# Optimization experiments

Hardware: AMD Instinct MI355X
Metric: run time of the kernel (lower is better)

Reference implementation:

```python
import jax, jax.numpy as jnp
import numpy as np

D_MODEL = 512
N_HEADS = 8
HEAD_DIM = D_MODEL // N_HEADS
MAX_LEN = 250  # relative table has 2*MAX_LEN-1 = 499 rows
B, L = 2, 2048


def setup_inputs() -> dict:
    rng = jax.random.key(0)
    ks = jax.random.split(rng, 10)
    w = 1.0 / np.sqrt(D_MODEL)
    return {
        "query": jax.random.normal(ks[0], (B, L, D_MODEL), jnp.float32),
        "key": jax.random.normal(ks[1], (B, L, D_MODEL), jnp.float32),
        "value": jax.random.normal(ks[2], (B, L, D_MODEL), jnp.float32),
        "mask": jax.random.randint(ks[3], (B, L), 0, 2, jnp.int32),
        # weights stored as [in, out]; apply as x @ W + b (equivalent to torch Linear)
        "Wq": jax.random.normal(ks[4], (D_MODEL, D_MODEL), jnp.float32) * w,
        "bq": jnp.zeros((D_MODEL,), jnp.float32),
        "Wk": jax.random.normal(ks[5], (D_MODEL, D_MODEL), jnp.float32) * w,
        "bk": jnp.zeros((D_MODEL,), jnp.float32),
        "Wv": jax.random.normal(ks[6], (D_MODEL, D_MODEL), jnp.float32) * w,
        "bv": jnp.zeros((D_MODEL,), jnp.float32),
        "Wo": jax.random.normal(ks[7], (D_MODEL, D_MODEL), jnp.float32) * w,
        "bo": jnp.zeros((D_MODEL,), jnp.float32),
        "rel_table": jax.random.normal(ks[8], (2 * MAX_LEN - 1, HEAD_DIM), jnp.float32),
    }


def reference(query, key, value, mask, Wq, bq, Wk, bk, Wv, bv, Wo, bo, rel_table):
    b, l, d = query.shape
    hd = d // N_HEADS

    def split_heads(x):  # [b,l,d] -> [b,h,l,hd]
        return x.reshape(b, l, N_HEADS, hd).transpose(0, 2, 1, 3)

    Q = split_heads(query @ Wq + bq)
    K = split_heads(key @ Wk + bk)
    V = split_heads(value @ Wv + bv)

    scores = jnp.einsum('bhid,bhjd->bhij', Q, K) / jnp.sqrt(jnp.float32(hd))

    # relative position indices: idx[i,j] = clamp(j - i + MAX_LEN-1, 0, 2*MAX_LEN-2)
    pos = jnp.arange(l)
    idx = jnp.clip(pos[None, :] - pos[:, None] + MAX_LEN - 1, 0, 2 * MAX_LEN - 2)
    rel = rel_table[idx]  # [l, l, hd] gather
    # Shaw-style additive relative-position bias (per-pair scalar from Q . rel)
    scores = scores + jnp.einsum('bhid,ijd->bhij', Q, rel)

    # key-padding mask: [b,l] -> [b,1,1,l]
    scores = jnp.where(mask[:, None, None, :] == 0, jnp.float32(-1e10), scores)

    weights = jax.nn.softmax(scores, axis=-1)  # [b,h,l,l]
    out = jnp.einsum('bhij,bhjd->bhid', weights, V)
    out = out.transpose(0, 2, 1, 3).reshape(b, l, d)
    return out @ Wo + bo
```

## Files before the change

kernel.cpp:

```cpp
#include <hip/hip_runtime.h>
#include <math.h>

#define NREL 499
#define NREL_PAD 500
#define LDB 72
#define LDT 72

typedef __attribute__((ext_vector_type(8))) short bf16x8;
typedef __attribute__((ext_vector_type(4))) float f32x4;

__device__ __forceinline__ float bf2f(ushort x) {
  union { unsigned u; float f; } v; v.u = ((unsigned)x) << 16; return v.f;
}
__device__ __forceinline__ ushort f2bf(float x) {
  union { float f; unsigned u; } v; v.f = x;
  return (ushort)((v.u + 0x8000u) >> 16);
}
__device__ __forceinline__ bf16x8 pack8(float4 a, float4 b) {
  bf16x8 r;
  r[0] = (short)f2bf(a.x); r[1] = (short)f2bf(a.y);
  r[2] = (short)f2bf(a.z); r[3] = (short)f2bf(a.w);
  r[4] = (short)f2bf(b.x); r[5] = (short)f2bf(b.y);
  r[6] = (short)f2bf(b.z); r[7] = (short)f2bf(b.w);
  return r;
}

__global__ __launch_bounds__(256) void prep_wt(const float* __restrict__ W0,
                                               const float* __restrict__ W1,
                                               const float* __restrict__ W2,
                                               const float* __restrict__ W3,
                                               const int* __restrict__ mask,
                                               ushort* __restrict__ Wt,
                                               ushort* __restrict__ maskbf) {
  __shared__ float T[64][68];
  const int t = threadIdx.x;
  const int k0 = blockIdx.x * 64, n0 = blockIdx.y * 64, z = blockIdx.z;
  const float* W = (z == 0) ? W0 : (z == 1) ? W1 : (z == 2) ? W2 : W3;
#pragma unroll
  for (int s = 0; s < 4; ++s) {
    int idx = t + s * 256;
    int r = idx >> 4, c4 = (idx & 15) << 2;
    *(float4*)&T[r][c4] = *(const float4*)(W + (size_t)(k0 + r) * 512 + n0 + c4);
  }
  if (blockIdx.x == 0 && blockIdx.y == 0) {
    int base = z * 1024 + t * 4;
    int4 mv = *(const int4*)(mask + base);
    ushort4 mo;
    mo.x = mv.x ? 0x3F80 : 0; mo.y = mv.y ? 0x3F80 : 0;
    mo.z = mv.z ? 0x3F80 : 0; mo.w = mv.w ? 0x3F80 : 0;
    *(ushort4*)(maskbf + base) = mo;
  }
  __syncthreads();
#pragma unroll
  for (int s = 0; s < 4; ++s) {
    int idx = t + s * 256;
    int row = idx >> 4, c4 = (idx & 15) << 2;
    ushort4 u = make_ushort4(f2bf(T[c4 + 0][row]), f2bf(T[c4 + 1][row]),
                             f2bf(T[c4 + 2][row]), f2bf(T[c4 + 3][row]));
    *(ushort4*)(Wt + (size_t)z * 262144 + (size_t)(n0 + row) * 512 + k0 + c4) = u;
  }
}

template <int MODE, int AFP32>
__device__ __forceinline__ void gemm_tile_body(const void* __restrict__ Av,
                                               const ushort* __restrict__ Wt,
                                               const float* __restrict__ bias,
                                               const int* __restrict__ mvec,
                                               void* __restrict__ outv,
                                               int bx, int by, float oscale) {
  __shared__ ushort As[64 * LDT];
  __shared__ ushort Bs[64 * LDT];
  const int t = threadIdx.x;
  const int lane = t & 63, wave = t >> 6;
  const int m16 = lane & 15, quad = lane >> 4;
  const int koff = quad << 3;
  const int i0 = by * 64, n0 = bx * 64;
  const int row0 = t >> 3, off0 = (t & 7) << 3;
  const int row1 = (t + 256) >> 3, off1 = ((t + 256) & 7) << 3;
  const ushort* Ab16 = (const ushort*)Av + (size_t)i0 * 512;
  const float*  Ab32 = (const float*)Av + (size_t)i0 * 512;
  const ushort* Bb = Wt + (size_t)n0 * 512;

  uint4 ar0, ar1;
  float4 af00, af01, af10, af11;
  if (AFP32) {
    af00 = *(const float4*)(Ab32 + (size_t)row0 * 512 + off0);
    af01 = *(const float4*)(Ab32 + (size_t)row0 * 512 + off0 + 4);
    af10 = *(const float4*)(Ab32 + (size_t)row1 * 512 + off1);
    af11 = *(const float4*)(Ab32 + (size_t)row1 * 512 + off1 + 4);
  } else {
    ar0 = *(const uint4*)(Ab16 + (size_t)row0 * 512 + off0);
    ar1 = *(const uint4*)(Ab16 + (size_t)row1 * 512 + off1);
  }
  uint4 br0 = *(const uint4*)(Bb + (size_t)row0 * 512 + off0);
  uint4 br1 = *(const uint4*)(Bb + (size_t)row1 * 512 + off1);

  f32x4 acc[4] = {{0.f, 0.f, 0.f, 0.f}, {0.f, 0.f, 0.f, 0.f},
                  {0.f, 0.f, 0.f, 0.f}, {0.f, 0.f, 0.f, 0.f}};

  for (int ks = 0; ks < 8; ++ks) {
    __syncthreads();
    if (AFP32) {
      *(bf16x8*)&As[row0 * LDT + off0] = pack8(af00, af01);
      *(bf16x8*)&As[row1 * LDT + off1] = pack8(af10, af11);
    } else {
      *(uint4*)&As[row0 * LDT + off0] = ar0;
      *(uint4*)&As[row1 * LDT + off1] = ar1;
    }
    *(uint4*)&Bs[row0 * LDT + off0] = br0;
    *(uint4*)&Bs[row1 * LDT + off1] = br1;
    __syncthreads();

    const int kn = ((ks + 1) & 7) << 6;
    if (AFP32) {
      af00 = *(const float4*)(Ab32 + (size_t)row0 * 512 + kn + off0);
      af01 = *(const float4*)(Ab32 + (size_t)row0 * 512 + kn + off0 + 4);
      af10 = *(const float4*)(Ab32 + (size_t)row1 * 512 + kn + off1);
      af11 = *(const float4*)(Ab32 + (size_t)row1 * 512 + kn + off1 + 4);
    } else {
      ar0 = *(const uint4*)(Ab16 + (size_t)row0 * 512 + kn + off0);
      ar1 = *(const uint4*)(Ab16 + (size_t)row1 * 512 + kn + off1);
    }
    br0 = *(const uint4*)(Bb + (size_t)row0 * 512 + kn + off0);
    br1 = *(const uint4*)(Bb + (size_t)row1 * 512 + kn + off1);

    __builtin_amdgcn_s_setprio(1);
    if (MODE != 1) {
#pragma unroll
      for (int kh = 0; kh < 2; ++kh) {
        bf16x8 af = *(const bf16x8*)&As[((wave << 4) + m16) * LDT + (kh << 5) + koff];
#pragma unroll
        for (int nt = 0; nt < 4; ++nt) {
          bf16x8 wf = *(const bf16x8*)&Bs[((nt << 4) + m16) * LDT + (kh << 5) + koff];
          acc[nt] = __builtin_amdgcn_mfma_f32_16x16x32_bf16(af, wf, acc[nt], 0, 0, 0);
        }
      }
    } else {
#pragma unroll
      for (int kh = 0; kh < 2; ++kh) {
        bf16x8 wf = *(const bf16x8*)&Bs[((wave << 4) + m16) * LDT + (kh << 5) + koff];
#pragma unroll
        for (int it = 0; it < 4; ++it) {
          bf16x8 af = *(const bf16x8*)&As[((it << 4) + m16) * LDT + (kh << 5) + koff];
          acc[it] = __builtin_amdgcn_mfma_f32_16x16x32_bf16(wf, af, acc[it], 0, 0, 0);
        }
      }
    }
    __builtin_amdgcn_s_setprio(0);
  }

  if (MODE == 0) {
    float* out = (float*)outv;
#pragma unroll
    for (int nt = 0; nt < 4; ++nt) {
      float bn = bias[n0 + (nt << 4) + m16];
#pragma unroll
      for (int r = 0; r < 4; ++r) {
        int i = i0 + (wave << 4) + (quad << 2) + r;
        out[(size_t)i * 512 + n0 + (nt << 4) + m16] = acc[nt][r] + bn;
      }
    }
  } else if (MODE == 2) {
    ushort* out = (ushort*)outv;
    const int b = i0 >> 11, l0 = i0 & 2047, h = n0 >> 6;
#pragma unroll
    for (int nt = 0; nt < 4; ++nt) {
      float bn = bias[n0 + (nt << 4) + m16];
      int d = (nt << 4) + m16;
#pragma unroll
      for (int r = 0; r < 4; ++r) {
        int il = (wave << 4) + (quad << 2) + r;
        out[((size_t)(b * 8 + h) * 2048 + l0 + il) * 64 + d] =
            f2bf((acc[nt][r] + bn) * oscale);
      }
    }
  } else {
    ushort* out = (ushort*)outv;
    const int b = i0 >> 11, l0 = i0 & 2047, h = n0 >> 6;
    float4 b4 = *(const float4*)(bias + n0 + (wave << 4) + (quad << 2));
    float bb[4] = {b4.x, b4.y, b4.z, b4.w};
    float mkf[4];
#pragma unroll
    for (int it = 0; it < 4; ++it)
      mkf[it] = (mvec[b * 2048 + l0 + (it << 4) + m16] != 0) ? 1.f : 0.f;
#pragma unroll
    for (int r = 0; r < 4; ++r) {
      int d = (wave << 4) + (quad << 2) + r;
#pragma unroll
      for (int it = 0; it < 4; ++it) {
        out[((size_t)(b * 8 + h) * 64 + d) * 2048 + l0 + (it << 4) + m16] =
            f2bf((acc[it][r] + bb[r]) * mkf[it]);
      }
    }
  }
}

template <int MODE, int AFP32>
__global__ __launch_bounds__(256) void gemm_tile(const void* __restrict__ A,
                                                 const ushort* __restrict__ Wt,
                                                 const float* __restrict__ bias,
                                                 void* __restrict__ outv) {
  gemm_tile_body<MODE, AFP32>(A, Wt, bias, nullptr, outv, blockIdx.x,
                              blockIdx.y, 1.f);
}

__global__ __launch_bounds__(256) void gemm_qkv(
    const float* __restrict__ q, const float* __restrict__ k,
    const float* __restrict__ v, const ushort* __restrict__ Wt,
    const float* __restrict__ bq, const float* __restrict__ bk,
    const float* __restrict__ bv, const int* __restrict__ mask,
    ushort* __restrict__ Qw, ushort* __restrict__ Kw, ushort* __restrict__ Vtw) {
  const int z = blockIdx.z;
  if (z == 0) {
    gemm_tile_body<2, 1>(q, Wt, bq, nullptr, (void*)Qw, blockIdx.x, blockIdx.y,
                         0.125f);
  } else if (z == 1) {
    gemm_tile_body<2, 1>(k, Wt + 262144, bk, nullptr, (void*)Kw, blockIdx.x,
                         blockIdx.y, 1.f);
  } else {
    gemm_tile_body<1, 1>(v, Wt + 2 * 262144, bv, mask, (void*)Vtw, blockIdx.x,
                         blockIdx.y, 1.f);
  }
}

__global__ __launch_bounds__(256) void qrel_mfma(const ushort* __restrict__ Qw,
                                                 const float* __restrict__ rel,
                                                 float* __restrict__ qrel) {
  const int t = threadIdx.x;
  const int lane = t & 63, wave = t >> 6;
  const int m16 = lane & 15, quad = lane >> 4;
  const int r0 = blockIdx.x * 64;
  const int i0 = blockIdx.y * 64;
  const int bh = blockIdx.z;
  const ushort* Qb = Qw + ((size_t)bh * 2048 + i0 + (wave << 4) + m16) * 64;
  bf16x8 qa0 = *(const bf16x8*)(Qb + (quad << 3));
  bf16x8 qa1 = *(const bf16x8*)(Qb + 32 + (quad << 3));

  f32x4 acc[4] = {{0.f, 0.f, 0.f, 0.f}, {0.f, 0.f, 0.f, 0.f},
                  {0.f, 0.f, 0.f, 0.f}, {0.f, 0.f, 0.f, 0.f}};
#pragma unroll
  for (int rt = 0; rt < 4; ++rt) {
    int rr = min(r0 + (rt << 4) + m16, NREL - 1);
    const float* rp = rel + (size_t)rr * 64 + (quad << 3);
    float4 a0 = *(const float4*)rp,        a1 = *(const float4*)(rp + 4);
    float4 a2 = *(const float4*)(rp + 32), a3 = *(const float4*)(rp + 36);
    a0.x *= 8.f; a0.y *= 8.f; a0.z *= 8.f; a0.w *= 8.f;
    a1.x *= 8.f; a1.y *= 8.f; a1.z *= 8.f; a1.w *= 8.f;
    a2.x *= 8.f; a2.y *= 8.f; a2.z *= 8.f; a2.w *= 8.f;
    a3.x *= 8.f; a3.y *= 8.f; a3.z *= 8.f; a3.w *= 8.f;
    bf16x8 rf0 = pack8(a0, a1);
    bf16x8 rf1 = pack8(a2, a3);
    acc[rt] = __builtin_amdgcn_mfma_f32_16x16x32_bf16(qa0, rf0, acc[rt], 0, 0, 0);
    acc[rt] = __builtin_amdgcn_mfma_f32_16x16x32_bf16(qa1, rf1, acc[rt], 0, 0, 0);
  }
#pragma unroll
  for (int rt = 0; rt < 4; ++rt) {
    int r = r0 + (rt << 4) + m16;
    if (r < NREL_PAD) {
#pragma unroll
      for (int rg = 0; rg < 4; ++rg) {
        int i = i0 + (wave << 4) + (quad << 2) + rg;
        qrel[((size_t)bh * 2048 + i) * NREL_PAD + r] = acc[rt][rg];
      }
    }
  }
}

__device__ __forceinline__ void gather_qv(float qv[4][4],
                                          const float* __restrict__ qrow,
                                          float e_lo, float e_hi,
                                          int iq, int iw0, int j0, int quad) {
  if (j0 - iw0 >= 264) {
#pragma unroll
    for (int jt = 0; jt < 4; ++jt)
#pragma unroll
      for (int r = 0; r < 4; ++r) qv[jt][r] = e_hi;
  } else if (iw0 - j0 >= 312) {
#pragma unroll
    for (int jt = 0; jt < 4; ++jt)
#pragma unroll
      for (int r = 0; r < 4; ++r) qv[jt][r] = e_lo;
  } else {
#pragma unroll
    for (int jt = 0; jt < 4; ++jt) {
#pragma unroll
      for (int r = 0; r < 4; ++r) {
        int j = j0 + (jt << 4) + (quad << 2) + r;
        int rr = min(NREL - 1, max(0, j - iq + 249));
        qv[jt][r] = qrow[rr];
      }
    }
  }
}

template <int SPLIT>
__global__ __launch_bounds__(256) void flash_attn(
    const ushort* __restrict__ Qw, const ushort* __restrict__ Kw,
    const ushort* __restrict__ Vt, const float* __restrict__ qrel,
    const ushort* __restrict__ maskbf, ushort* __restrict__ attnbf,
    float* __restrict__ Opart, float* __restrict__ MLp) {
  __shared__ ushort QPs[64 * LDB];
  __shared__ ushort Ks[64 * LDB];
  __shared__ ushort Vs[64 * LDB];
  const int t = threadIdx.x;
  const int lane = t & 63, wave = t >> 6;
  const int m16 = lane & 15, quad = lane >> 4;
  const int koff = quad << 3;
  const int bid = ((int)blockIdx.y << 5) + (int)blockIdx.x;
  const int swz = ((bid & 7) << 6) + (bid >> 3);
  const int i0 = (swz & 31) << 6;
  const int bh = swz >> 5;
  const int b = bh >> 3, h = bh & 7;
  const int jstart = SPLIT ? ((int)blockIdx.z << 10) : 0;
  const int jend = SPLIT ? (jstart + 1024) : 2048;
  const ushort* Qb = Qw + (size_t)bh * 2048 * 64;
  const ushort* Kb = Kw + (size_t)bh * 2048 * 64;
  const ushort* Vb = Vt + (size_t)bh * 64 * 2048;
  const ushort* mbf = maskbf + b * 2048;
  const int iw0 = i0 + (wave << 4);
  const int iq = iw0 + m16;
  const float* qrow = qrel + ((size_t)bh * 2048 + iq) * NREL_PAD;
  const float e_lo = qrow[0], e_hi = qrow[NREL - 1];

  const int row0 = t >> 3, off0 = (t & 7) << 3;
  const int row1 = (t + 256) >> 3, off1 = ((t + 256) & 7) << 3;

  *(uint4*)&QPs[row0 * LDB + off0] =
      *(const uint4*)(Qb + (size_t)(i0 + row0) * 64 + off0);
  *(uint4*)&QPs[row1 * LDB + off1] =
      *(const uint4*)(Qb + (size_t)(i0 + row1) * 64 + off1);
  __syncthreads();

  bf16x8 qa0 = *(const bf16x8*)&QPs[((wave << 4) + m16) * LDB + koff];
  bf16x8 qa1 = *(const bf16x8*)&QPs[((wave << 4) + m16) * LDB + 32 + koff];

  uint4 kr0 = *(const uint4*)(Kb + (size_t)(jstart + row0) * 64 + off0);
  uint4 kr1 = *(const uint4*)(Kb + (size_t)(jstart + row1) * 64 + off1);
  uint4 vr0 = *(const uint4*)(Vb + (size_t)row0 * 2048 + jstart + off0);
  uint4 vr1 = *(const uint4*)(Vb + (size_t)row1 * 2048 + jstart + off1);
  bf16x8 mfr0 = *(const bf16x8*)(mbf + jstart + koff);
  bf16x8 mfr1 = *(const bf16x8*)(mbf + jstart + 32 + koff);
  float qv[4][4];
  gather_qv(qv, qrow, e_lo, e_hi, iq, iw0, jstart, quad);

  float m_i = -INFINITY;
  f32x4 oacc[4];
  f32x4 lacc = {0.f, 0.f, 0.f, 0.f};
#pragma unroll
  for (int dt = 0; dt < 4; ++dt) oacc[dt] = (f32x4){0.f, 0.f, 0.f, 0.f};

  for (int j0 = jstart; j0 < jend; j0 += 64) {
    __syncthreads();
    *(uint4*)&Ks[row0 * LDB + off0] = kr0;
    *(uint4*)&Ks[row1 * LDB + off1] = kr1;
    *(uint4*)&Vs[row0 * LDB + off0] = vr0;
    *(uint4*)&Vs[row1 * LDB + off1] = vr1;
    __syncthreads();

    const int jn = (j0 + 64 < jend) ? (j0 + 64) : jstart;
    uint4 kn0 = *(const uint4*)(Kb + (size_t)(jn + row0) * 64 + off0);
    uint4 kn1 = *(const uint4*)(Kb + (size_t)(jn + row1) * 64 + off1);
    uint4 vn0 = *(const uint4*)(Vb + (size_t)row0 * 2048 + jn + off0);
    uint4 vn1 = *(const uint4*)(Vb + (size_t)row1 * 2048 + jn + off1);
    bf16x8 mfn0 = *(const bf16x8*)(mbf + jn + koff);
    bf16x8 mfn1 = *(const bf16x8*)(mbf + jn + 32 + koff);
    float qn[4][4];
    gather_qv(qn, qrow, e_lo, e_hi, iq, iw0, jn, quad);

    f32x4 sacc[4];
    __builtin_amdgcn_s_setprio(1);
#pragma unroll
    for (int jt = 0; jt < 4; ++jt) {
      bf16x8 kb0 = *(const bf16x8*)&Ks[((jt << 4) + m16) * LDB + koff];
      bf16x8 kb1 = *(const bf16x8*)&Ks[((jt << 4) + m16) * LDB + 32 + koff];
      f32x4 z = {qv[jt][0], qv[jt][1], qv[jt][2], qv[jt][3]};
      z = __builtin_amdgcn_mfma_f32_16x16x32_bf16(kb0, qa0, z, 0, 0, 0);
      z = __builtin_amdgcn_mfma_f32_16x16x32_bf16(kb1, qa1, z, 0, 0, 0);
      sacc[jt] = z;
    }
    __builtin_amdgcn_s_setprio(0);

    float t0 = fmaxf(fmaxf(sacc[0][0], sacc[0][1]), fmaxf(sacc[0][2], sacc[0][3]));
    float t1 = fmaxf(fmaxf(sacc[1][0], sacc[1][1]), fmaxf(sacc[1][2], sacc[1][3]));
    float t2 = fmaxf(fmaxf(sacc[2][0], sacc[2][1]), fmaxf(sacc[2][2], sacc[2][3]));
    float t3 = fmaxf(fmaxf(sacc[3][0], sacc[3][1]), fmaxf(sacc[3][2], sacc[3][3]));
    float mx = fmaxf(fmaxf(t0, t1), fmaxf(t2, t3));
    mx = fmaxf(mx, __shfl_xor(mx, 16));
    mx = fmaxf(mx, __shfl_xor(mx, 32));

    if (__any(mx > m_i + 8.f)) {
      float mnew = fmaxf(m_i, mx);
      float al = __expf(m_i - mnew);
      m_i = mnew;
#pragma unroll
      for (int dt = 0; dt < 4; ++dt)
#pragma unroll
        for (int r = 0; r < 4; ++r) oacc[dt][r] *= al;
#pragma unroll
      for (int r = 0; r < 4; ++r) lacc[r] *= al;
    }

    const int prow = ((wave << 4) + m16) * LDB;
#pragma unroll
    for (int jt = 0; jt < 4; ++jt) {
      ushort4 pk;
      pk.x = f2bf(__expf(sacc[jt][0] - m_i));
      pk.y = f2bf(__expf(sacc[jt][1] - m_i));
      pk.z = f2bf(__expf(sacc[jt][2] - m_i));
      pk.w = f2bf(__expf(sacc[jt][3] - m_i));
      *(ushort4*)&QPs[prow + (jt << 4) + (quad << 2)] = pk;
    }
    __asm__ volatile("s_waitcnt lgkmcnt(0)" ::: "memory");

    bf16x8 pa0 = *(const bf16x8*)&QPs[prow + koff];
    bf16x8 pa1 = *(const bf16x8*)&QPs[prow + 32 + koff];
    __builtin_amdgcn_s_setprio(1);
    lacc = __builtin_amdgcn_mfma_f32_16x16x32_bf16(mfr0, pa0, lacc, 0, 0, 0);
    lacc = __builtin_amdgcn_mfma_f32_16x16x32_bf16(mfr1, pa1, lacc, 0, 0, 0);
#pragma unroll
    for (int dt = 0; dt < 4; ++dt) {
      bf16x8 vb0 = *(const bf16x8*)&Vs[((dt << 4) + m16) * LDB + koff];
      bf16x8 vb1 = *(const bf16x8*)&Vs[((dt << 4) + m16) * LDB + 32 + koff];
      oacc[dt] = __builtin_amdgcn_mfma_f32_16x16x32_bf16(vb0, pa0, oacc[dt], 0, 0, 0);
      oacc[dt] = __builtin_amdgcn_mfma_f32_16x16x32_bf16(vb1, pa1, oacc[dt], 0, 0, 0);
    }
    __builtin_amdgcn_s_setprio(0);

    kr0 = kn0; kr1 = kn1; vr0 = vn0; vr1 = vn1;
    mfr0 = mfn0; mfr1 = mfn1;
#pragma unroll
    for (int jt = 0; jt < 4; ++jt)
#pragma unroll
      for (int r = 0; r < 4; ++r) qv[jt][r] = qn[jt][r];
  }

  if (SPLIT) {
    const size_t rb = ((size_t)(((int)blockIdx.z << 4) + bh) * 2048 + iq);
    float* dst = Opart + rb * 64;
#pragma unroll
    for (int dt = 0; dt < 4; ++dt) {
      float4 st;
      st.x = oacc[dt][0]; st.y = oacc[dt][1];
      st.z = oacc[dt][2]; st.w = oacc[dt][3];
      *(float4*)(dst + (dt << 4) + (quad << 2)) = st;
    }
    if (quad == 0) { MLp[rb * 2] = m_i; MLp[rb * 2 + 1] = lacc[0]; }
  } else {
    float inv = 1.0f / lacc[0];
    ushort* dst = attnbf + (size_t)(b * 2048 + iq) * 512 + h * 64;
#pragma unroll
    for (int dt = 0; dt < 4; ++dt) {
      ushort4 st;
      st.x = f2bf(oacc[dt][0] * inv);
      st.y = f2bf(oacc[dt][1] * inv);
      st.z = f2bf(oacc[dt][2] * inv);
      st.w = f2bf(oacc[dt][3] * inv);
      *(ushort4*)(dst + (dt << 4) + (quad << 2)) = st;
    }
  }
}

__global__ __launch_bounds__(256) void combine_attn(
    const float* __restrict__ Opart, const float* __restrict__ MLp,
    ushort* __restrict__ attnbf) {
  const int t = threadIdx.x;
  const int i0 = blockIdx.x * 64, bh = blockIdx.y;
  const int b = bh >> 3, h = bh & 7;
  const int row = t >> 2, d0 = (t & 3) << 4;
  const int i = i0 + row;
  const size_t rb0 = (size_t)bh * 2048 + i;
  const size_t rb1 = (size_t)(16 + bh) * 2048 + i;
  float m0 = MLp[rb0 * 2], l0 = MLp[rb0 * 2 + 1];
  float m1 = MLp[rb1 * 2], l1 = MLp[rb1 * 2 + 1];
  float M = fmaxf(m0, m1);
  float w0 = __expf(m0 - M), w1 = __expf(m1 - M);
  float inv = 1.0f / (w0 * l0 + w1 * l1);
  const float* p0 = Opart + rb0 * 64 + d0;
  const float* p1 = Opart + rb1 * 64 + d0;
  ushort* dst = attnbf + ((size_t)(b * 2048) + i) * 512 + h * 64 + d0;
#pragma unroll
  for (int c = 0; c < 4; ++c) {
    float4 a = *(const float4*)(p0 + c * 4);
    float4 q = *(const float4*)(p1 + c * 4);
    ushort4 o;
    o.x = f2bf((w0 * a.x + w1 * q.x) * inv);
    o.y = f2bf((w0 * a.y + w1 * q.y) * inv);
    o.z = f2bf((w0 * a.z + w1 * q.z) * inv);
    o.w = f2bf((w0 * a.w + w1 * q.w) * inv);
    *(ushort4*)(dst + c * 4) = o;
  }
}

extern "C" void kernel_launch(void* const* d_in, const int* in_sizes, int n_in,
                              void* d_out, int out_size, void* d_ws,
                              size_t ws_size, hipStream_t stream) {
  const float* query = (const float*)d_in[0];
  const float* key   = (const float*)d_in[1];
  const float* value = (const float*)d_in[2];
  const int*   mask  = (const int*)d_in[3];
  const float* Wq = (const float*)d_in[4];
  const float* bq = (const float*)d_in[5];
  const float* Wk = (const float*)d_in[6];
  const float* bk = (const float*)d_in[7];
  const float* Wv = (const float*)d_in[8];
  const float* bv = (const float*)d_in[9];
  const float* Wo = (const float*)d_in[10];
  const float* bo = (const float*)d_in[11];
  const float* rel = (const float*)d_in[12];

  char* w = (char*)d_ws;
  size_t off = 0;
  ushort* Qw  = (ushort*)(w + off); off += (size_t)16 * 2048 * 64 * 2;
  ushort* Kw  = (ushort*)(w + off); off += (size_t)16 * 2048 * 64 * 2;
  ushort* Vtw = (ushort*)(w + off); off += (size_t)16 * 64 * 2048 * 2;
  ushort* Wt  = (ushort*)(w + off); off += (size_t)4 * 512 * 512 * 2;
  float* qrel = (float*)(w + off);  off += (size_t)16 * 2048 * NREL_PAD * 4;
  ushort* attnbf = (ushort*)(w + off); off += (size_t)4096 * 512 * 2;
  ushort* maskbf = (ushort*)(w + off); off += (size_t)2 * 2048 * 2 + 8160;
  float* Opart = (float*)(w + off); off += (size_t)2 * 16 * 2048 * 64 * 4;
  float* MLp  = (float*)(w + off);  off += (size_t)2 * 16 * 2048 * 2 * 4;
  float* out = (float*)d_out;
  const bool split = (ws_size >= off);

  dim3 bb(256);
  hipLaunchKernelGGL(prep_wt, dim3(8, 8, 4), bb, 0, stream, Wq, Wk, Wv, Wo,
                     mask, Wt, maskbf);
  hipLaunchKernelGGL(gemm_qkv, dim3(8, 64, 3), bb, 0, stream, query, key, value,
                     Wt, bq, bk, bv, mask, Qw, Kw, Vtw);
  hipLaunchKernelGGL(qrel_mfma, dim3(8, 32, 16), bb, 0, stream, Qw, rel, qrel);
  if (split) {
    hipLaunchKernelGGL((flash_attn<1>), dim3(32, 16, 2), bb, 0, stream, Qw, Kw,
                       Vtw, qrel, maskbf, attnbf, Opart, MLp);
    hipLaunchKernelGGL(combine_attn, dim3(32, 16), bb, 0, stream, Opart, MLp,
                       attnbf);
  } else {
    hipLaunchKernelGGL((flash_attn<0>), dim3(32, 16), bb, 0, stream, Qw, Kw,
                       Vtw, qrel, maskbf, attnbf, (float*)attnbf,
                       (float*)attnbf);
  }
  hipLaunchKernelGGL((gemm_tile<0, 0>), dim3(8, 64), bb, 0, stream, attnbf,
                     Wt + 3 * 262144, bo, (void*)out);
}
```

Measured before the change: 242.6 us.

## Drop split-KV flash attention and stage bf16 rel table through LDS in qrel

Precomputes a bf16, pre-scaled copy of the relative-position table in the weight-prep kernel. The qrel kernel then loads Q and rel tiles into shared memory with coalesced loads, replacing per-lane fp32 loads and conversions. The split-KV flash attention path and its combine kernel are removed in favour of a single unsplit pass, eliminating the partial-output writes and the extra launch. The trade-off is half as many attention blocks, which may reduce GPU occupancy.

```diff
diff --git a/kernel.cpp b/kernel.cpp
--- a/kernel.cpp
+++ b/kernel.cpp
@@ -30,8 +30,10 @@
                                                const float* __restrict__ W2,
                                                const float* __restrict__ W3,
                                                const int* __restrict__ mask,
+                                               const float* __restrict__ rel,
                                                ushort* __restrict__ Wt,
-                                               ushort* __restrict__ maskbf) {
+                                               ushort* __restrict__ maskbf,
+                                               ushort* __restrict__ rel8) {
   __shared__ float T[64][68];
   const int t = threadIdx.x;
   const int k0 = blockIdx.x * 64, n0 = blockIdx.y * 64, z = blockIdx.z;
@@ -49,6 +51,22 @@
     mo.x = mv.x ? 0x3F80 : 0; mo.y = mv.y ? 0x3F80 : 0;
     mo.z = mv.z ? 0x3F80 : 0; mo.w = mv.w ? 0x3F80 : 0;
     *(ushort4*)(maskbf + base) = mo;
+  } else if (blockIdx.x == 1 && blockIdx.y == 0) {
+    int base = z * 8192 + t * 32;
+#pragma unroll
+    for (int c = 0; c < 4; ++c) {
+      ushort4 o;
+      int e0 = base + c * 8;
+      ushort tmp[8];
+#pragma unroll
+      for (int k = 0; k < 8; ++k) {
+        int e = e0 + k;
+        float v = (e < NREL * 64) ? rel[e] * 8.f : 0.f;
+        tmp[k] = f2bf(v);
+      }
+      *(ushort4*)(rel8 + e0) = make_ushort4(tmp[0], tmp[1], tmp[2], tmp[3]);
+      *(ushort4*)(rel8 + e0 + 4) = make_ushort4(tmp[4], tmp[5], tmp[6], tmp[7]);
+    }
   }
   __syncthreads();
 #pragma unroll
@@ -223,44 +241,51 @@
   }
 }
 
-__global__ __launch_bounds__(256) void qrel_mfma(const ushort* __restrict__ Qw,
-                                                 const float* __restrict__ rel,
+__global__ __launch_bounds__(256) void qrel_tile(const ushort* __restrict__ Qw,
+                                                 const ushort* __restrict__ rel8,
                                                  float* __restrict__ qrel) {
+  __shared__ ushort As[64 * LDT];
+  __shared__ ushort Bs[64 * LDT];
   const int t = threadIdx.x;
   const int lane = t & 63, wave = t >> 6;
   const int m16 = lane & 15, quad = lane >> 4;
+  const int koff = quad << 3;
   const int r0 = blockIdx.x * 64;
   const int i0 = blockIdx.y * 64;
   const int bh = blockIdx.z;
-  const ushort* Qb = Qw + ((size_t)bh * 2048 + i0 + (wave << 4) + m16) * 64;
-  bf16x8 qa0 = *(const bf16x8*)(Qb + (quad << 3));
-  bf16x8 qa1 = *(const bf16x8*)(Qb + 32 + (quad << 3));
+  const int row0 = t >> 3, off0 = (t & 7) << 3;
+  const int row1 = (t + 256) >> 3, off1 = ((t + 256) & 7) << 3;
+
+  *(uint4*)&As[row0 * LDT + off0] =
+      *(const uint4*)(Qw + ((size_t)bh * 2048 + i0 + row0) * 64 + off0);
+  *(uint4*)&As[row1 * LDT + off1] =
+      *(const uint4*)(Qw + ((size_t)bh * 2048 + i0 + row1) * 64 + off1);
+  *(uint4*)&Bs[row0 * LDT + off0] =
+      *(const uint4*)(rel8 + (size_t)(r0 + row0) * 64 + off0);
+  *(uint4*)&Bs[row1 * LDT + off1] =
+      *(const uint4*)(rel8 + (size_t)(r0 + row1) * 64 + off1);
+  __syncthreads();
 
   f32x4 acc[4] = {{0.f, 0.f, 0.f, 0.f}, {0.f, 0.f, 0.f, 0.f},
                   {0.f, 0.f, 0.f, 0.f}, {0.f, 0.f, 0.f, 0.f}};
 #pragma unroll
-  for (int rt = 0; rt < 4; ++rt) {
-    int rr = min(r0 + (rt << 4) + m16, NREL - 1);
-    const float* rp = rel + (size_t)rr * 64 + (quad << 3);
-    float4 a0 = *(const float4*)rp,        a1 = *(const float4*)(rp + 4);
-    float4 a2 = *(const float4*)(rp + 32), a3 = *(const float4*)(rp + 36);
-    a0.x *= 8.f; a0.y *= 8.f; a0.z *= 8.f; a0.w *= 8.f;
-    a1.x *= 8.f; a1.y *= 8.f; a1.z *= 8.f; a1.w *= 8.f;
-    a2.x *= 8.f; a2.y *= 8.f; a2.z *= 8.f; a2.w *= 8.f;
-    a3.x *= 8.f; a3.y *= 8.f; a3.z *= 8.f; a3.w *= 8.f;
-    bf16x8 rf0 = pack8(a0, a1);
-    bf16x8 rf1 = pack8(a2, a3);
-    acc[rt] = __builtin_amdgcn_mfma_f32_16x16x32_bf16(qa0, rf0, acc[rt], 0, 0, 0);
-    acc[rt] = __builtin_amdgcn_mfma_f32_16x16x32_bf16(qa1, rf1, acc[rt], 0, 0, 0);
-  }
-#pragma unroll
-  for (int rt = 0; rt < 4; ++rt) {
-    int r = r0 + (rt << 4) + m16;
+  for (int kh = 0; kh < 2; ++kh) {
+    bf16x8 af = *(const bf16x8*)&As[((wave << 4) + m16) * LDT + (kh << 5) + koff];
+#pragma unroll
+    for (int nt = 0; nt < 4; ++nt) {
+      bf16x8 wf = *(const bf16x8*)&Bs[((nt << 4) + m16) * LDT + (kh << 5) + koff];
+      acc[nt] = __builtin_amdgcn_mfma_f32_16x16x32_bf16(af, wf, acc[nt], 0, 0, 0);
+    }
+  }
+
+#pragma unroll
+  for (int nt = 0; nt < 4; ++nt) {
+    int r = r0 + (nt << 4) + m16;
     if (r < NREL_PAD) {
 #pragma unroll
       for (int rg = 0; rg < 4; ++rg) {
         int i = i0 + (wave << 4) + (quad << 2) + rg;
-        qrel[((size_t)bh * 2048 + i) * NREL_PAD + r] = acc[rt][rg];
+        qrel[((size_t)bh * 2048 + i) * NREL_PAD + r] = acc[nt][rg];
       }
     }
   }
@@ -293,12 +318,10 @@
   }
 }
 
-template <int SPLIT>
 __global__ __launch_bounds__(256) void flash_attn(
     const ushort* __restrict__ Qw, const ushort* __restrict__ Kw,
     const ushort* __restrict__ Vt, const float* __restrict__ qrel,
-    const ushort* __restrict__ maskbf, ushort* __restrict__ attnbf,
-    float* __restrict__ Opart, float* __restrict__ MLp) {
+    const ushort* __restrict__ maskbf, ushort* __restrict__ attnbf) {
   __shared__ ushort QPs[64 * LDB];
   __shared__ ushort Ks[64 * LDB];
   __shared__ ushort Vs[64 * LDB];
@@ -311,8 +334,6 @@
   const int i0 = (swz & 31) << 6;
   const int bh = swz >> 5;
   const int b = bh >> 3, h = bh & 7;
-  const int jstart = SPLIT ? ((int)blockIdx.z << 10) : 0;
-  const int jend = SPLIT ? (jstart + 1024) : 2048;
   const ushort* Qb = Qw + (size_t)bh * 2048 * 64;
   const ushort* Kb = Kw + (size_t)bh * 2048 * 64;
   const ushort* Vb = Vt + (size_t)bh * 64 * 2048;
@@ -334,14 +355,14 @@
   bf16x8 qa0 = *(const bf16x8*)&QPs[((wave << 4) + m16) * LDB + koff];
   bf16x8 qa1 = *(const bf16x8*)&QPs[((wave << 4) + m16) * LDB + 32 + koff];
 
-  uint4 kr0 = *(const uint4*)(Kb + (size_t)(jstart + row0) * 64 + off0);
-  uint4 kr1 = *(const uint4*)(Kb + (size_t)(jstart + row1) * 64 + off1);
-  uint4 vr0 = *(const uint4*)(Vb + (size_t)row0 * 2048 + jstart + off0);
-  uint4 vr1 = *(const uint4*)(Vb + (size_t)row1 * 2048 + jstart + off1);
-  bf16x8 mfr0 = *(const bf16x8*)(mbf + jstart + koff);
-  bf16x8 mfr1 = *(const bf16x8*)(mbf + jstart + 32 + koff);
+  uint4 kr0 = *(const uint4*)(Kb + (size_t)row0 * 64 + off0);
+  uint4 kr1 = *(const uint4*)(Kb + (size_t)row1 * 64 + off1);
+  uint4 vr0 = *(const uint4*)(Vb + (size_t)row0 * 2048 + off0);
+  uint4 vr1 = *(const uint4*)(Vb + (size_t)row1 * 2048 + off1);
+  bf16x8 mfr0 = *(const bf16x8*)(mbf + koff);
+  bf16x8 mfr1 = *(const bf16x8*)(mbf + 32 + koff);
   float qv[4][4];
-  gather_qv(qv, qrow, e_lo, e_hi, iq, iw0, jstart, quad);
+  gather_qv(qv, qrow, e_lo, e_hi, iq, iw0, 0, quad);
 
   float m_i = -INFINITY;
   f32x4 oacc[4];
@@ -349,7 +370,7 @@
 #pragma unroll
   for (int dt = 0; dt < 4; ++dt) oacc[dt] = (f32x4){0.f, 0.f, 0.f, 0.f};
 
-  for (int j0 = jstart; j0 < jend; j0 += 64) {
+  for (int j0 = 0; j0 < 2048; j0 += 64) {
     __syncthreads();
     *(uint4*)&Ks[row0 * LDB + off0] = kr0;
     *(uint4*)&Ks[row1 * LDB + off1] = kr1;
@@ -357,7 +378,7 @@
     *(uint4*)&Vs[row1 * LDB + off1] = vr1;
     __syncthreads();
 
-    const int jn = (j0 + 64 < jend) ? (j0 + 64) : jstart;
+    const int jn = (j0 + 64) & 2047;
     uint4 kn0 = *(const uint4*)(Kb + (size_t)(jn + row0) * 64 + off0);
     uint4 kn1 = *(const uint4*)(Kb + (size_t)(jn + row1) * 64 + off1);
     uint4 vn0 = *(const uint4*)(Vb + (size_t)row0 * 2048 + jn + off0);
@@ -434,60 +455,16 @@
       for (int r = 0; r < 4; ++r) qv[jt][r] = qn[jt][r];
   }
 
-  if (SPLIT) {
-    const size_t rb = ((size_t)(((int)blockIdx.z << 4) + bh) * 2048 + iq);
-    float* dst = Opart + rb * 64;
-#pragma unroll
-    for (int dt = 0; dt < 4; ++dt) {
-      float4 st;
-      st.x = oacc[dt][0]; st.y = oacc[dt][1];
-      st.z = oacc[dt][2]; st.w = oacc[dt][3];
-      *(float4*)(dst + (dt << 4) + (quad << 2)) = st;
-    }
-    if (quad == 0) { MLp[rb * 2] = m_i; MLp[rb * 2 + 1] = lacc[0]; }
-  } else {
-    float inv = 1.0f / lacc[0];
-    ushort* dst = attnbf + (size_t)(b * 2048 + iq) * 512 + h * 64;
-#pragma unroll
-    for (int dt = 0; dt < 4; ++dt) {
-      ushort4 st;
-      st.x = f2bf(oacc[dt][0] * inv);
-      st.y = f2bf(oacc[dt][1] * inv);
-      st.z = f2bf(oacc[dt][2] * inv);
-      st.w = f2bf(oacc[dt][3] * inv);
-      *(ushort4*)(dst + (dt << 4) + (quad << 2)) = st;
-    }
-  }
-}
-
-__global__ __launch_bounds__(256) void combine_attn(
-    const float* __restrict__ Opart, const float* __restrict__ MLp,
-    ushort* __restrict__ attnbf) {
-  const int t = threadIdx.x;
-  const int i0 = blockIdx.x * 64, bh = blockIdx.y;
-  const int b = bh >> 3, h = bh & 7;
-  const int row = t >> 2, d0 = (t & 3) << 4;
-  const int i = i0 + row;
-  const size_t rb0 = (size_t)bh * 2048 + i;
-  const size_t rb1 = (size_t)(16 + bh) * 2048 + i;
-  float m0 = MLp[rb0 * 2], l0 = MLp[rb0 * 2 + 1];
-  float m1 = MLp[rb1 * 2], l1 = MLp[rb1 * 2 + 1];
-  float M = fmaxf(m0, m1);
-  float w0 = __expf(m0 - M), w1 = __expf(m1 - M);
-  float inv = 1.0f / (w0 * l0 + w1 * l1);
-  const float* p0 = Opart + rb0 * 64 + d0;
-  const float* p1 = Opart + rb1 * 64 + d0;
-  ushort* dst = attnbf + ((size_t)(b * 2048) + i) * 512 + h * 64 + d0;
-#pragma unroll
-  for (int c = 0; c < 4; ++c) {
-    float4 a = *(const float4*)(p0 + c * 4);
-    float4 q = *(const float4*)(p1 + c * 4);
-    ushort4 o;
-    o.x = f2bf((w0 * a.x + w1 * q.x) * inv);
-    o.y = f2bf((w0 * a.y + w1 * q.y) * inv);
-    o.z = f2bf((w0 * a.z + w1 * q.z) * inv);
-    o.w = f2bf((w0 * a.w + w1 * q.w) * inv);
-    *(ushort4*)(dst + c * 4) = o;
+  float inv = 1.0f / lacc[0];
+  ushort* dst = attnbf + (size_t)(b * 2048 + iq) * 512 + h * 64;
+#pragma unroll
+  for (int dt = 0; dt < 4; ++dt) {
+    ushort4 st;
+    st.x = f2bf(oacc[dt][0] * inv);
+    st.y = f2bf(oacc[dt][1] * inv);
+    st.z = f2bf(oacc[dt][2] * inv);
+    st.w = f2bf(oacc[dt][3] * inv);
+    *(ushort4*)(dst + (dt << 4) + (quad << 2)) = st;
   }
 }
 
@@ -516,28 +493,18 @@
   ushort* Wt  = (ushort*)(w + off); off += (size_t)4 * 512 * 512 * 2;
   float* qrel = (float*)(w + off);  off += (size_t)16 * 2048 * NREL_PAD * 4;
   ushort* attnbf = (ushort*)(w + off); off += (size_t)4096 * 512 * 2;
-  ushort* maskbf = (ushort*)(w + off); off += (size_t)2 * 2048 * 2 + 8160;
-  float* Opart = (float*)(w + off); off += (size_t)2 * 16 * 2048 * 64 * 4;
-  float* MLp  = (float*)(w + off);  off += (size_t)2 * 16 * 2048 * 2 * 4;
+  ushort* maskbf = (ushort*)(w + off); off += (size_t)2 * 2048 * 2;
+  ushort* rel8 = (ushort*)(w + off); off += (size_t)512 * 64 * 2;
   float* out = (float*)d_out;
-  const bool split = (ws_size >= off);
 
   dim3 bb(256);
   hipLaunchKernelGGL(prep_wt, dim3(8, 8, 4), bb, 0, stream, Wq, Wk, Wv, Wo,
-                     mask, Wt, maskbf);
+                     mask, rel, Wt, maskbf, rel8);
   hipLaunchKernelGGL(gemm_qkv, dim3(8, 64, 3), bb, 0, stream, query, key, value,
                      Wt, bq, bk, bv, mask, Qw, Kw, Vtw);
-  hipLaunchKernelGGL(qrel_mfma, dim3(8, 32, 16), bb, 0, stream, Qw, rel, qrel);
-  if (split) {
-    hipLaunchKernelGGL((flash_attn<1>), dim3(32, 16, 2), bb, 0, stream, Qw, Kw,
-                       Vtw, qrel, maskbf, attnbf, Opart, MLp);
-    hipLaunchKernelGGL(combine_attn, dim3(32, 16), bb, 0, stream, Opart, MLp,
-                       attnbf);
-  } else {
-    hipLaunchKernelGGL((flash_attn<0>), dim3(32, 16), bb, 0, stream, Qw, Kw,
-                       Vtw, qrel, maskbf, attnbf, (float*)attnbf,
-                       (float*)attnbf);
-  }
+  hipLaunchKernelGGL(qrel_tile, dim3(8, 32, 16), bb, 0, stream, Qw, rel8, qrel);
+  hipLaunchKernelGGL(flash_attn, dim3(32, 16), bb, 0, stream, Qw, Kw, Vtw, qrel,
+                     maskbf, attnbf);
   hipLaunchKernelGGL((gemm_tile<0, 0>), dim3(8, 64), bb, 0, stream, attnbf,
                      Wt + 3 * 262144, bo, (void*)out);
 }
```

After: 219.1 us. -9.7%, faster.
